# Performance work log

Measured on AMD Instinct MI355X. Metric: run time of the kernel, lower is better.

Reference implementation:

```python
import jax, jax.numpy as jnp
import numpy as np

DIM = 512
B, QL, KL = 8, 1024, 4096

def setup_inputs() -> dict:
    key = jax.random.key(0)
    k1, k2, k3 = jax.random.split(key, 3)
    output = jax.random.normal(k1, (B, QL, DIM), dtype=jnp.float32)
    context = jax.random.normal(k2, (B, KL, DIM), dtype=jnp.float32)
    # nn.Linear(2*dim, dim): weight [dim, 2*dim]; store transposed [2*dim, dim]
    W_out = jax.random.normal(k3, (DIM, 2 * DIM), dtype=jnp.float32) * (1.0 / np.sqrt(2 * DIM))
    b_out = jnp.zeros((DIM,), dtype=jnp.float32)
    return {"output": output, "context": context, "W_out": W_out, "b_out": b_out}

def reference(output, context, W_out, b_out):
    # scores: [B, QL, KL]
    attn = jnp.einsum("bqd,bkd->bqk", output, context)
    attn = jax.nn.softmax(attn, axis=-1)
    # mix: [B, QL, D]
    mix = jnp.einsum("bqk,bkd->bqd", attn, context)
    combined = jnp.concatenate([mix, output], axis=-1)  # [B, QL, 2D]
    out = jnp.tanh(jnp.einsum("bqe,de->bqd", combined, W_out) + b_out)
    return (out, attn)
```

## Files before the change

### kernel.cpp

```cpp
#include <hip/hip_runtime.h>
#include <math.h>

#define DIMM 512
#define NB 8
#define QLEN 1024
#define KLEN 4096

typedef __attribute__((ext_vector_type(4))) float floatx4;
typedef __attribute__((ext_vector_type(8))) short short8;
typedef __attribute__((ext_vector_type(4))) unsigned short ushort4v;
typedef __attribute__((ext_vector_type(8))) unsigned short ushort8v;

static __device__ __forceinline__ unsigned short f2bf(float f) {
    unsigned u = __builtin_bit_cast(unsigned, f);
    u += 0x7FFFu + ((u >> 16) & 1u);
    return (unsigned short)(u >> 16);
}
static __device__ __forceinline__ float bf2f(unsigned short h) {
    unsigned u = ((unsigned)h) << 16;
    return __builtin_bit_cast(float, u);
}

static __device__ __forceinline__ void gload16(const unsigned short* g, unsigned short* l) {
    __builtin_amdgcn_global_load_lds(
        (__attribute__((address_space(1))) void*)const_cast<unsigned short*>(g),
        (__attribute__((address_space(3))) void*)l,
        16, 0, 0);
}

__global__ __launch_bounds__(256) void split_k(const float* __restrict__ x,
                                               unsigned short* __restrict__ dst) {
    int idx = blockIdx.x * 256 + threadIdx.x;
    float4 v = ((const float4*)x)[idx];
    int r = idx >> 7;
    int c = (idx & 127) << 2;
    float f[4] = {v.x, v.y, v.z, v.w};
    ushort4v hi, lo;
#pragma unroll
    for (int e = 0; e < 4; ++e) {
        unsigned short h = f2bf(f[e]);
        hi[e] = h;
        lo[e] = f2bf(f[e] - bf2f(h));
    }
    unsigned short* row = dst + ((size_t)r << 10);
    *(ushort4v*)(row + c) = hi;
    *(ushort4v*)(row + 512 + c) = lo;
}

__global__ __launch_bounds__(256) void conv_hi(const float* __restrict__ x,
                                               unsigned short* __restrict__ dst,
                                               int c4shift, int ldd, int off) {
    int idx = blockIdx.x * 256 + threadIdx.x;
    float4 v = ((const float4*)x)[idx];
    int r = idx >> c4shift;
    int c = (idx & ((1 << c4shift) - 1)) << 2;
    ushort4v hi;
    hi[0] = f2bf(v.x); hi[1] = f2bf(v.y); hi[2] = f2bf(v.z); hi[3] = f2bf(v.w);
    *(ushort4v*)(dst + (size_t)r * ldd + off + c) = hi;
}

__global__ __launch_bounds__(256) void trans_hi(const float* __restrict__ ctx,
                                                unsigned short* __restrict__ ctxT) {
    __shared__ unsigned short tile[64][66];
    int b = blockIdx.z;
    int c0 = blockIdx.x * 64;
    int k0 = blockIdx.y * 64;
    const float* src = ctx + ((size_t)b * KLEN + k0) * DIMM + c0;
    int t = threadIdx.x;
    int rr = t >> 4, cc4 = (t & 15) * 4;
#pragma unroll
    for (int it = 0; it < 4; ++it) {
        int r = rr + it * 16;
        float4 v = *(const float4*)(src + (size_t)r * DIMM + cc4);
        tile[r][cc4 + 0] = f2bf(v.x);
        tile[r][cc4 + 1] = f2bf(v.y);
        tile[r][cc4 + 2] = f2bf(v.z);
        tile[r][cc4 + 3] = f2bf(v.w);
    }
    __syncthreads();
#pragma unroll
    for (int it = 0; it < 2; ++it) {
        int u = t + it * 256;
        int c = u >> 3;
        int kk = (u & 7) * 8;
        ushort8v o;
#pragma unroll
        for (int e = 0; e < 8; ++e) o[e] = tile[kk + e][c];
        *(ushort8v*)(ctxT + ((size_t)b * DIMM + c0 + c) * KLEN + k0 + kk) = o;
    }
}

__global__ __launch_bounds__(256) void softmax_k(float* __restrict__ S,
                                                 unsigned short* __restrict__ Pb) {
    size_t row = blockIdx.x;
    float* p = S + row * KLEN;
    int t = threadIdx.x;
    int lane = t & 63, wv = t >> 6;
    float4 v[4];
    float mx = -3.0e38f;
#pragma unroll
    for (int i = 0; i < 4; ++i) {
        v[i] = *(const float4*)(p + i * 1024 + t * 4);
        mx = fmaxf(mx, fmaxf(fmaxf(v[i].x, v[i].y), fmaxf(v[i].z, v[i].w)));
    }
#pragma unroll
    for (int m = 32; m >= 1; m >>= 1) mx = fmaxf(mx, __shfl_xor(mx, m, 64));
    __shared__ float redm[4], reds[4];
    if (lane == 0) redm[wv] = mx;
    __syncthreads();
    mx = fmaxf(fmaxf(redm[0], redm[1]), fmaxf(redm[2], redm[3]));
    float sum = 0.f;
#pragma unroll
    for (int i = 0; i < 4; ++i) {
        v[i].x = __expf(v[i].x - mx); v[i].y = __expf(v[i].y - mx);
        v[i].z = __expf(v[i].z - mx); v[i].w = __expf(v[i].w - mx);
        sum += v[i].x + v[i].y + v[i].z + v[i].w;
    }
#pragma unroll
    for (int m = 32; m >= 1; m >>= 1) sum += __shfl_xor(sum, m, 64);
    if (lane == 0) reds[wv] = sum;
    __syncthreads();
    float inv = 1.0f / (reds[0] + reds[1] + reds[2] + reds[3]);
    unsigned short* pb = Pb + row * KLEN;
#pragma unroll
    for (int i = 0; i < 4; ++i) {
        float4 w;
        w.x = v[i].x * inv; w.y = v[i].y * inv; w.z = v[i].z * inv; w.w = v[i].w * inv;
        *(float4*)(p + i * 1024 + t * 4) = w;
        ushort4v h;
        h[0] = f2bf(w.x); h[1] = f2bf(w.y); h[2] = f2bf(w.z); h[3] = f2bf(w.w);
        *(ushort4v*)(pb + i * 1024 + t * 4) = h;
    }
}

template <int EPI, bool REMAP>
__global__ __launch_bounds__(256) void gemm_bt(
    const unsigned short* __restrict__ A,
    const unsigned short* __restrict__ Bm,
    float* __restrict__ Cf, unsigned short* __restrict__ Cb,
    const float* __restrict__ bias,
    int Ktiles, long lda, long ldb, long ldc,
    long a_bs, long b_bs, long c_bs) {
    __shared__ unsigned short sA[128 * 64];
    __shared__ unsigned short sB[128 * 64];
    const int tid = threadIdx.x;
    const int lane = tid & 63;
    const int wv = tid >> 6;
    const int wm = wv >> 1, wn = wv & 1;
    const int mlane = lane & 15, quad = lane >> 4;
    const unsigned short* Ab = A + (size_t)blockIdx.z * a_bs + (size_t)blockIdx.y * 128 * lda;
    const unsigned short* Bb = Bm + (size_t)blockIdx.z * b_bs + (size_t)blockIdx.x * 128 * ldb;
    const int r8 = tid >> 3;
    const int c8 = (tid & 7) << 3;
    unsigned short* la = sA + r8 * 64 + c8;
    unsigned short* lb = sB + r8 * 64 + c8;

    floatx4 acc[4][4] = {};

    for (int kt = 0; kt < Ktiles; ++kt) {
        long kv = (long)kt * 64;
        long ka = REMAP ? (kv >= 512 ? kv - 512 : kv) : kv;
        long kb = REMAP ? (kv >= 1024 ? kv - 1024 : kv) : kv;
        if (kt) __syncthreads();
        const unsigned short* ga = Ab + (size_t)r8 * lda + ka + c8;
        const unsigned short* gb = Bb + (size_t)r8 * ldb + kb + c8;
#pragma unroll
        for (int it = 0; it < 4; ++it) {
            gload16(ga + (size_t)(it * 32) * lda, la + it * 2048);
            gload16(gb + (size_t)(it * 32) * ldb, lb + it * 2048);
        }
        __syncthreads();
#pragma unroll
        for (int s = 0; s < 2; ++s) {
            short8 af[4], bf[4];
#pragma unroll
            for (int i = 0; i < 4; ++i)
                af[i] = *(const short8*)(sA + (wm * 64 + i * 16 + mlane) * 64 + s * 32 + quad * 8);
#pragma unroll
            for (int j = 0; j < 4; ++j)
                bf[j] = *(const short8*)(sB + (wn * 64 + j * 16 + mlane) * 64 + s * 32 + quad * 8);
#pragma unroll
            for (int i = 0; i < 4; ++i)
#pragma unroll
                for (int j = 0; j < 4; ++j)
                    acc[i][j] = __builtin_amdgcn_mfma_f32_16x16x32_bf16(af[i], bf[j], acc[i][j], 0, 0, 0);
        }
    }

    size_t crow0 = (size_t)blockIdx.y * 128 + wm * 64 + quad * 4;
    size_t ccol0 = (size_t)blockIdx.x * 128 + wn * 64 + mlane;
    size_t cbase = (size_t)blockIdx.z * c_bs;
#pragma unroll
    for (int i = 0; i < 4; ++i) {
#pragma unroll
        for (int j = 0; j < 4; ++j) {
            size_t gr = crow0 + i * 16;
            size_t gc = ccol0 + j * 16;
#pragma unroll
            for (int r = 0; r < 4; ++r) {
                float vv = acc[i][j][r];
                size_t off = cbase + (gr + r) * ldc + gc;
                if (EPI == 0) Cf[off] = vv;
                else if (EPI == 1) Cb[off] = f2bf(vv);
                else Cf[off] = tanhf(vv + bias[gc]);
            }
        }
    }
}

extern "C" void kernel_launch(void* const* d_in, const int* in_sizes, int n_in,
                              void* d_out, int out_size, void* d_ws, size_t ws_size,
                              hipStream_t stream) {
    (void)in_sizes; (void)n_in; (void)out_size; (void)ws_size;
    const float* outp = (const float*)d_in[0];
    const float* ctx  = (const float*)d_in[1];
    const float* W    = (const float*)d_in[2];
    const float* bias = (const float*)d_in[3];

    float* out0 = (float*)d_out;
    float* attn = out0 + (size_t)NB * QLEN * DIMM;

    unsigned char* w = (unsigned char*)d_ws;
    unsigned short* R1 = (unsigned short*)(w);
    unsigned short* R2 = (unsigned short*)(w + (16ull << 20));
    unsigned short* R3 = (unsigned short*)(w + (80ull << 20));
    unsigned short* R4 = (unsigned short*)(w + (112ull << 20));

    split_k<<<4096, 256, 0, stream>>>(outp, R1);
    split_k<<<16384, 256, 0, stream>>>(ctx, R2);
    trans_hi<<<dim3(8, 64, 8), 256, 0, stream>>>(ctx, R3);
    conv_hi<<<512, 256, 0, stream>>>(W, R4, 8, 1024, 0);

    gemm_bt<0, true><<<dim3(32, 8, 8), 256, 0, stream>>>(
        R1, R2, attn, nullptr, nullptr,
        24, 1024, 1024, 4096,
        (long)QLEN * 1024, (long)KLEN * 1024, (long)QLEN * KLEN);

    softmax_k<<<8192, 256, 0, stream>>>(attn, R2);

    conv_hi<<<4096, 256, 0, stream>>>(outp, R1, 7, 1024, 512);

    gemm_bt<1, false><<<dim3(4, 8, 8), 256, 0, stream>>>(
        R2, R3, nullptr, R1, nullptr,
        64, 4096, 4096, 1024,
        (long)QLEN * KLEN, (long)DIMM * KLEN, (long)QLEN * 1024);

    gemm_bt<2, false><<<dim3(4, 64, 1), 256, 0, stream>>>(
        R1, R4, out0, nullptr, bias,
        16, 1024, 1024, 512, 0, 0, 0);
}
```

Measured before the change: 543.2 us.

## XOR-swizzle GEMM LDS tiles and use narrower N tiles for small GEMMs

Applies an XOR swizzle to the LDS layout of the A and B tiles, both on the global-to-LDS load and on the MFMA fragment reads, to avoid LDS bank conflicts. The GEMM is templated on the N tile width, and the mix and output GEMMs switch to 64-wide N tiles. That doubles their block count (256 and 512 blocks) so more of the CUs are busy. The cost is lower operand reuse per block and more A-tile reloads.

```diff
diff --git a/kernel.cpp b/kernel.cpp
--- a/kernel.cpp
+++ b/kernel.cpp
@@ -133,7 +133,7 @@
     }
 }
 
-template <int EPI, bool REMAP>
+template <int EPI, bool REMAP, int BN>
 __global__ __launch_bounds__(256) void gemm_bt(
     const unsigned short* __restrict__ A,
     const unsigned short* __restrict__ Bm,
@@ -141,59 +141,63 @@
     const float* __restrict__ bias,
     int Ktiles, long lda, long ldb, long ldc,
     long a_bs, long b_bs, long c_bs) {
+    constexpr int NF = BN / 32;
     __shared__ unsigned short sA[128 * 64];
-    __shared__ unsigned short sB[128 * 64];
+    __shared__ unsigned short sB[BN * 64];
     const int tid = threadIdx.x;
     const int lane = tid & 63;
     const int wv = tid >> 6;
     const int wm = wv >> 1, wn = wv & 1;
     const int mlane = lane & 15, quad = lane >> 4;
     const unsigned short* Ab = A + (size_t)blockIdx.z * a_bs + (size_t)blockIdx.y * 128 * lda;
-    const unsigned short* Bb = Bm + (size_t)blockIdx.z * b_bs + (size_t)blockIdx.x * 128 * ldb;
+    const unsigned short* Bb = Bm + (size_t)blockIdx.z * b_bs + (size_t)blockIdx.x * BN * ldb;
     const int r8 = tid >> 3;
     const int c8 = (tid & 7) << 3;
+    const int cg = ((tid & 7) ^ ((tid >> 3) & 7)) << 3;
     unsigned short* la = sA + r8 * 64 + c8;
     unsigned short* lb = sB + r8 * 64 + c8;
 
-    floatx4 acc[4][4] = {};
+    floatx4 acc[4][NF] = {};
 
     for (int kt = 0; kt < Ktiles; ++kt) {
         long kv = (long)kt * 64;
         long ka = REMAP ? (kv >= 512 ? kv - 512 : kv) : kv;
         long kb = REMAP ? (kv >= 1024 ? kv - 1024 : kv) : kv;
         if (kt) __syncthreads();
-        const unsigned short* ga = Ab + (size_t)r8 * lda + ka + c8;
-        const unsigned short* gb = Bb + (size_t)r8 * ldb + kb + c8;
-#pragma unroll
-        for (int it = 0; it < 4; ++it) {
+        const unsigned short* ga = Ab + (size_t)r8 * lda + ka + cg;
+        const unsigned short* gb = Bb + (size_t)r8 * ldb + kb + cg;
+#pragma unroll
+        for (int it = 0; it < 4; ++it)
             gload16(ga + (size_t)(it * 32) * lda, la + it * 2048);
+#pragma unroll
+        for (int it = 0; it < BN / 32; ++it)
             gload16(gb + (size_t)(it * 32) * ldb, lb + it * 2048);
-        }
         __syncthreads();
 #pragma unroll
         for (int s = 0; s < 2; ++s) {
-            short8 af[4], bf[4];
+            const int swz = (((s * 4 + quad) ^ (mlane & 7)) << 3);
+            short8 af[4], bf[NF];
 #pragma unroll
             for (int i = 0; i < 4; ++i)
-                af[i] = *(const short8*)(sA + (wm * 64 + i * 16 + mlane) * 64 + s * 32 + quad * 8);
-#pragma unroll
-            for (int j = 0; j < 4; ++j)
-                bf[j] = *(const short8*)(sB + (wn * 64 + j * 16 + mlane) * 64 + s * 32 + quad * 8);
+                af[i] = *(const short8*)(sA + (wm * 64 + i * 16 + mlane) * 64 + swz);
+#pragma unroll
+            for (int j = 0; j < NF; ++j)
+                bf[j] = *(const short8*)(sB + (wn * (BN / 2) + j * 16 + mlane) * 64 + swz);
 #pragma unroll
             for (int i = 0; i < 4; ++i)
 #pragma unroll
-                for (int j = 0; j < 4; ++j)
+                for (int j = 0; j < NF; ++j)
                     acc[i][j] = __builtin_amdgcn_mfma_f32_16x16x32_bf16(af[i], bf[j], acc[i][j], 0, 0, 0);
         }
     }
 
     size_t crow0 = (size_t)blockIdx.y * 128 + wm * 64 + quad * 4;
-    size_t ccol0 = (size_t)blockIdx.x * 128 + wn * 64 + mlane;
+    size_t ccol0 = (size_t)blockIdx.x * BN + wn * (BN / 2) + mlane;
     size_t cbase = (size_t)blockIdx.z * c_bs;
 #pragma unroll
     for (int i = 0; i < 4; ++i) {
 #pragma unroll
-        for (int j = 0; j < 4; ++j) {
+        for (int j = 0; j < NF; ++j) {
             size_t gr = crow0 + i * 16;
             size_t gc = ccol0 + j * 16;
 #pragma unroll
@@ -231,7 +235,7 @@
     trans_hi<<<dim3(8, 64, 8), 256, 0, stream>>>(ctx, R3);
     conv_hi<<<512, 256, 0, stream>>>(W, R4, 8, 1024, 0);
 
-    gemm_bt<0, true><<<dim3(32, 8, 8), 256, 0, stream>>>(
+    gemm_bt<0, true, 128><<<dim3(32, 8, 8), 256, 0, stream>>>(
         R1, R2, attn, nullptr, nullptr,
         24, 1024, 1024, 4096,
         (long)QLEN * 1024, (long)KLEN * 1024, (long)QLEN * KLEN);
@@ -240,12 +244,12 @@
 
     conv_hi<<<4096, 256, 0, stream>>>(outp, R1, 7, 1024, 512);
 
-    gemm_bt<1, false><<<dim3(4, 8, 8), 256, 0, stream>>>(
+    gemm_bt<1, false, 64><<<dim3(8, 8, 8), 256, 0, stream>>>(
         R2, R3, nullptr, R1, nullptr,
         64, 4096, 4096, 1024,
         (long)QLEN * KLEN, (long)DIMM * KLEN, (long)QLEN * 1024);
 
-    gemm_bt<2, false><<<dim3(4, 64, 1), 256, 0, stream>>>(
+    gemm_bt<2, false, 64><<<dim3(8, 64, 1), 256, 0, stream>>>(
         R1, R4, out0, nullptr, bias,
         16, 1024, 1024, 512, 0, 0, 0);
 }
```

Result: faster. 505.5 us (-6.9%).
